# Kernel tuning notes

Measured on AMD Instinct MI355X. Metric: run time of the kernel, lower is better.

Reference implementation:

```python
import jax, jax.numpy as jnp
import numpy as np

# Hyperparameters (from __init__ defaults)
TIME_RES = 25
BASE_RES = 512
MAX_RES = 32768
N_LEVELS = 8
N_FEATS = 4
LOG2_HASHMAP = 13
HASHMAP_SIZE = 1 << LOG2_HASHMAP  # 8192
PRIME_Y = np.uint32(2654435761)   # instant-ngp 2D hash prime (dim0 prime is 1)

# Per-level grid scales (tcnn convention: scale = 2^(l*log2_pls)*base - 1)
_LOG2_PLS = np.log2(MAX_RES / BASE_RES) / (N_LEVELS - 1)
SCALES = jnp.asarray(np.exp2(np.arange(N_LEVELS) * _LOG2_PLS) * BASE_RES - 1.0,
                     dtype=jnp.float32)  # [L]


def _hash_encode(x, table_t):
    """Instant-NGP 2D multires hash encoding for one time slice.
    x: [N,2] in [0,1); table_t: [L, H, F]. Returns [N, L*F].
    All levels satisfy res^2 > HASHMAP_SIZE, so always the hash path."""
    N = x.shape[0]
    pos = x[:, None, :] * SCALES[None, :, None] + 0.5        # [N,L,2]
    pos_i = jnp.floor(pos)
    frac = pos - pos_i                                        # [N,L,2]
    pos_i = pos_i.astype(jnp.uint32)
    lvl = jnp.arange(N_LEVELS, dtype=jnp.int32)[None, :]      # [1,L]
    acc = jnp.zeros((N, N_LEVELS, N_FEATS), dtype=table_t.dtype)
    mask = jnp.uint32(HASHMAP_SIZE - 1)
    for dx in (0, 1):  # 4 bilinear corners (static unroll)
        for dy in (0, 1):
            ix = pos_i[..., 0] + jnp.uint32(dx)               # [N,L]
            iy = pos_i[..., 1] + jnp.uint32(dy)
            h = jnp.bitwise_xor(ix, iy * PRIME_Y) & mask      # [N,L] hash index
            w = (frac[..., 0] if dx else 1.0 - frac[..., 0]) * \
                (frac[..., 1] if dy else 1.0 - frac[..., 1])  # [N,L]
            f = table_t[lvl, h.astype(jnp.int32)]             # [N,L,F] gather
            acc = acc + w[..., None] * f
    return acc.reshape(N, N_LEVELS * N_FEATS)


def setup_inputs() -> dict:
    key = jax.random.key(0)
    k1, k2 = jax.random.split(key)
    N = 2_000_000
    x = jax.random.uniform(k1, (N, 2), dtype=jnp.float32)
    t = jnp.asarray(0.3, dtype=jnp.float32)  # scalar time in [0,1]
    # tcnn initializes hash tables uniform in [-1e-4, 1e-4]
    table = jax.random.uniform(k2, (TIME_RES, N_LEVELS, HASHMAP_SIZE, N_FEATS),
                               dtype=jnp.float32, minval=-1e-4, maxval=1e-4)
    return {"x": x, "t": t, "table": table}


def reference(x, t, table):
    idx = t * (TIME_RES - 1)
    i1 = jnp.floor(idx).astype(jnp.int32)
    i2 = jnp.ceil(idx).astype(jnp.int32)
    # blend weight; equals (i2-idx, idx-i1) when i1!=i2 and (1,0) when equal,
    # matching the torch branch semantics.
    w2 = idx - i1.astype(idx.dtype)
    w1 = 1.0 - w2
    tab1 = jax.lax.dynamic_index_in_dim(table, i1, axis=0, keepdims=False)
    tab2 = jax.lax.dynamic_index_in_dim(table, i2, axis=0, keepdims=False)
    f1 = _hash_encode(x, tab1)  # [N, 32]
    f2 = _hash_encode(x, tab2)
    return w1 * f1 + w2 * f2
```

## Files before the change

### kernel.cpp

```cpp
#include <hip/hip_runtime.h>
#include <hip/hip_fp16.h>
#include <math.h>

#define NLV 8
#define NF 4
#define HSZ 8192
#define TRES 25
#define PRIME 2654435761u

struct Scales { float s[NLV]; };

__global__ __launch_bounds__(256) void blend_kernel(
    const float* __restrict__ table, const float* __restrict__ tptr,
    __half2* __restrict__ bt)
{
    int i = blockIdx.x * 256 + threadIdx.x;
    float t = *tptr;
    float idx = t * (float)(TRES - 1);
    float fi1 = floorf(idx);
    float fi2 = ceilf(idx);
    float w2 = idx - fi1;
    float w1 = 1.0f - w2;
    size_t off1 = (size_t)(int)fi1 * (size_t)(NLV * HSZ * NF);
    size_t off2 = (size_t)(int)fi2 * (size_t)(NLV * HSZ * NF);
    float4 a = ((const float4*)(table + off1))[i];
    float4 b = ((const float4*)(table + off2))[i];
    float4 r;
    r.x = w1 * a.x + w2 * b.x;
    r.y = w1 * a.y + w2 * b.y;
    r.z = w1 * a.z + w2 * b.z;
    r.w = w1 * a.w + w2 * b.w;
    int l = i >> 13;
    int h = i & (HSZ - 1);
    bt[(size_t)l * 16384 + h]        = __floats2half2_rn(r.x, r.y);
    bt[(size_t)l * 16384 + 8192 + h] = __floats2half2_rn(r.z, r.w);
}

__global__ __launch_bounds__(1024) void encode_kernel(
    const float* __restrict__ x, const float4* __restrict__ bt,
    float* __restrict__ out, int npts, Scales sc)
{
    extern __shared__ __half2 smem[];
    int tid = threadIdx.x;
    int n0 = blockIdx.x * 1024 + tid;
    int n = n0 < npts ? n0 : npts - 1;
    float2 p = ((const float2*)x)[n];

    float4 acc[NLV];

    #pragma unroll
    for (int l = 0; l < NLV; ++l) {
        const float4* src = bt + (size_t)l * 4096;
        float4* dst = (float4*)smem;
        #pragma unroll
        for (int k = 0; k < 4; ++k) dst[tid + k * 1024] = src[tid + k * 1024];
        __syncthreads();

        float scale = sc.s[l];
        float px = __fadd_rn(__fmul_rn(p.x, scale), 0.5f);
        float py = __fadd_rn(__fmul_rn(p.y, scale), 0.5f);
        float fx0 = floorf(px), fy0 = floorf(py);
        float fx = px - fx0, fy = py - fy0;
        unsigned ix = (unsigned)(int)fx0;
        unsigned iy = (unsigned)(int)fy0;
        unsigned hy0 = iy * PRIME;
        unsigned hy1 = hy0 + PRIME;
        unsigned h00 = (ix         ^ hy0) & (HSZ - 1);
        unsigned h01 = (ix         ^ hy1) & (HSZ - 1);
        unsigned h10 = ((ix + 1u)  ^ hy0) & (HSZ - 1);
        unsigned h11 = ((ix + 1u)  ^ hy1) & (HSZ - 1);

        const __half2* t0 = smem;
        const __half2* t1 = smem + 8192;
        float2 a00 = __half22float2(t0[h00]), b00 = __half22float2(t1[h00]);
        float2 a01 = __half22float2(t0[h01]), b01 = __half22float2(t1[h01]);
        float2 a10 = __half22float2(t0[h10]), b10 = __half22float2(t1[h10]);
        float2 a11 = __half22float2(t0[h11]), b11 = __half22float2(t1[h11]);

        float gx = 1.0f - fx, gy = 1.0f - fy;
        float w00 = gx * gy, w01 = gx * fy, w10 = fx * gy, w11 = fx * fy;

        float4 r;
        r.x = w00 * a00.x + w01 * a01.x + w10 * a10.x + w11 * a11.x;
        r.y = w00 * a00.y + w01 * a01.y + w10 * a10.y + w11 * a11.y;
        r.z = w00 * b00.x + w01 * b01.x + w10 * b10.x + w11 * b11.x;
        r.w = w00 * b00.y + w01 * b01.y + w10 * b10.y + w11 * b11.y;
        acc[l] = r;
        __syncthreads();
    }

    if (n0 < npts) {
        float4* o = (float4*)(out + (size_t)n0 * 32);
        #pragma unroll
        for (int l = 0; l < NLV; ++l) o[l] = acc[l];
    }
}

extern "C" void kernel_launch(void* const* d_in, const int* in_sizes, int n_in,
                              void* d_out, int out_size, void* d_ws, size_t ws_size,
                              hipStream_t stream) {
    const float* x     = (const float*)d_in[0];
    const float* t     = (const float*)d_in[1];
    const float* table = (const float*)d_in[2];
    float* out = (float*)d_out;
    __half2* bt = (__half2*)d_ws;

    int npts = in_sizes[0] / 2;

    Scales sc;
    const double l2p = log2(32768.0 / 512.0) / 7.0;
    for (int l = 0; l < NLV; ++l)
        sc.s[l] = (float)(exp2((double)l * l2p) * 512.0 - 1.0);

    blend_kernel<<<(NLV * HSZ) / 256, 256, 0, stream>>>(table, t, bt);

    int nblocks = (npts + 1023) / 1024;
    encode_kernel<<<nblocks, 1024, 64 * 1024, stream>>>(
        x, (const float4*)bt, out, npts, sc);
}
```

Before: 397.3 us.

## Process four points per thread with double-buffered interleaved LDS table

Each block now handles 4096 points, with each thread computing four points. The per-level table staged in LDS is reused across four times more points, cutting global/L2 reloads of the table. The level tables are double-buffered so the next level's global loads overlap the current gathers, leaving one barrier per level. The blend output is interleaved so each corner fetch is a single 8-byte LDS read. The 128KB static shared footprint limits occupancy to one block per CU and raises register pressure.

```diff
diff --git a/kernel.cpp b/kernel.cpp
--- a/kernel.cpp
+++ b/kernel.cpp
@@ -30,69 +30,116 @@
     r.y = w1 * a.y + w2 * b.y;
     r.z = w1 * a.z + w2 * b.z;
     r.w = w1 * a.w + w2 * b.w;
-    int l = i >> 13;
-    int h = i & (HSZ - 1);
-    bt[(size_t)l * 16384 + h]        = __floats2half2_rn(r.x, r.y);
-    bt[(size_t)l * 16384 + 8192 + h] = __floats2half2_rn(r.z, r.w);
+    bt[2 * (size_t)i]     = __floats2half2_rn(r.x, r.y);
+    bt[2 * (size_t)i + 1] = __floats2half2_rn(r.z, r.w);
 }
 
-__global__ __launch_bounds__(1024) void encode_kernel(
+__device__ __forceinline__ float2 h2f(unsigned u) {
+    return __half22float2(__builtin_bit_cast(__half2, u));
+}
+
+__device__ __forceinline__ float4 gather_lvl(const uint2* tbl, float2 p, float scale)
+{
+    float px = __fadd_rn(__fmul_rn(p.x, scale), 0.5f);
+    float py = __fadd_rn(__fmul_rn(p.y, scale), 0.5f);
+    float fx0 = floorf(px), fy0 = floorf(py);
+    float fx = px - fx0, fy = py - fy0;
+    unsigned ix = (unsigned)(int)fx0;
+    unsigned iy = (unsigned)(int)fy0;
+    unsigned hy0 = iy * PRIME;
+    unsigned hy1 = hy0 + PRIME;
+    unsigned h00 = (ix         ^ hy0) & (HSZ - 1);
+    unsigned h01 = (ix         ^ hy1) & (HSZ - 1);
+    unsigned h10 = ((ix + 1u)  ^ hy0) & (HSZ - 1);
+    unsigned h11 = ((ix + 1u)  ^ hy1) & (HSZ - 1);
+    uint2 v00 = tbl[h00];
+    uint2 v01 = tbl[h01];
+    uint2 v10 = tbl[h10];
+    uint2 v11 = tbl[h11];
+    float gx = 1.0f - fx, gy = 1.0f - fy;
+    float w00 = gx * gy, w01 = gx * fy, w10 = fx * gy, w11 = fx * fy;
+    float2 a00 = h2f(v00.x), b00 = h2f(v00.y);
+    float2 a01 = h2f(v01.x), b01 = h2f(v01.y);
+    float2 a10 = h2f(v10.x), b10 = h2f(v10.y);
+    float2 a11 = h2f(v11.x), b11 = h2f(v11.y);
+    float4 r;
+    r.x = w00 * a00.x + w01 * a01.x + w10 * a10.x + w11 * a11.x;
+    r.y = w00 * a00.y + w01 * a01.y + w10 * a10.y + w11 * a11.y;
+    r.z = w00 * b00.x + w01 * b01.x + w10 * b10.x + w11 * b11.x;
+    r.w = w00 * b00.y + w01 * b01.y + w10 * b10.y + w11 * b11.y;
+    return r;
+}
+
+__global__ __launch_bounds__(1024, 4) void encode_kernel(
     const float* __restrict__ x, const float4* __restrict__ bt,
     float* __restrict__ out, int npts, Scales sc)
 {
-    extern __shared__ __half2 smem[];
+    __shared__ float4 smem[2][4096];
     int tid = threadIdx.x;
-    int n0 = blockIdx.x * 1024 + tid;
-    int n = n0 < npts ? n0 : npts - 1;
-    float2 p = ((const float2*)x)[n];
+    int base = blockIdx.x * 4096 + tid;
+    int n0 = base, n1 = base + 1024, n2 = base + 2048, n3 = base + 3072;
+    int c0 = n0 < npts ? n0 : npts - 1;
+    int c1 = n1 < npts ? n1 : npts - 1;
+    int c2 = n2 < npts ? n2 : npts - 1;
+    int c3 = n3 < npts ? n3 : npts - 1;
+    float2 p0 = ((const float2*)x)[c0];
+    float2 p1 = ((const float2*)x)[c1];
+    float2 p2 = ((const float2*)x)[c2];
+    float2 p3 = ((const float2*)x)[c3];
 
-    float4 acc[NLV];
+    float4 acc[4][4];
+
+    {
+        const float4* src = bt;
+        float4 s0 = src[tid], s1 = src[tid + 1024],
+               s2 = src[tid + 2048], s3 = src[tid + 3072];
+        smem[0][tid] = s0; smem[0][tid + 1024] = s1;
+        smem[0][tid + 2048] = s2; smem[0][tid + 3072] = s3;
+    }
+    __syncthreads();
 
     #pragma unroll
     for (int l = 0; l < NLV; ++l) {
-        const float4* src = bt + (size_t)l * 4096;
-        float4* dst = (float4*)smem;
-        #pragma unroll
-        for (int k = 0; k < 4; ++k) dst[tid + k * 1024] = src[tid + k * 1024];
+        float4 s0, s1, s2, s3;
+        if (l < NLV - 1) {
+            const float4* src = bt + (size_t)(l + 1) * 4096;
+            s0 = src[tid];        s1 = src[tid + 1024];
+            s2 = src[tid + 2048]; s3 = src[tid + 3072];
+        }
+
+        const uint2* tbl = (const uint2*)smem[l & 1];
+        float scale = sc.s[l];
+        acc[0][l & 3] = gather_lvl(tbl, p0, scale);
+        acc[1][l & 3] = gather_lvl(tbl, p1, scale);
+        acc[2][l & 3] = gather_lvl(tbl, p2, scale);
+        acc[3][l & 3] = gather_lvl(tbl, p3, scale);
+
+        if (l < NLV - 1) {
+            float4* dst = smem[(l & 1) ^ 1];
+            dst[tid] = s0; dst[tid + 1024] = s1;
+            dst[tid + 2048] = s2; dst[tid + 3072] = s3;
+        }
+
+        if ((l & 3) == 3) {
+            int g = l >> 2;
+            if (n0 < npts) {
+                float4* o = (float4*)(out + (size_t)n0 * 32) + g * 4;
+                o[0] = acc[0][0]; o[1] = acc[0][1]; o[2] = acc[0][2]; o[3] = acc[0][3];
+            }
+            if (n1 < npts) {
+                float4* o = (float4*)(out + (size_t)n1 * 32) + g * 4;
+                o[0] = acc[1][0]; o[1] = acc[1][1]; o[2] = acc[1][2]; o[3] = acc[1][3];
+            }
+            if (n2 < npts) {
+                float4* o = (float4*)(out + (size_t)n2 * 32) + g * 4;
+                o[0] = acc[2][0]; o[1] = acc[2][1]; o[2] = acc[2][2]; o[3] = acc[2][3];
+            }
+            if (n3 < npts) {
+                float4* o = (float4*)(out + (size_t)n3 * 32) + g * 4;
+                o[0] = acc[3][0]; o[1] = acc[3][1]; o[2] = acc[3][2]; o[3] = acc[3][3];
+            }
+        }
         __syncthreads();
-
-        float scale = sc.s[l];
-        float px = __fadd_rn(__fmul_rn(p.x, scale), 0.5f);
-        float py = __fadd_rn(__fmul_rn(p.y, scale), 0.5f);
-        float fx0 = floorf(px), fy0 = floorf(py);
-        float fx = px - fx0, fy = py - fy0;
-        unsigned ix = (unsigned)(int)fx0;
-        unsigned iy = (unsigned)(int)fy0;
-        unsigned hy0 = iy * PRIME;
-        unsigned hy1 = hy0 + PRIME;
-        unsigned h00 = (ix         ^ hy0) & (HSZ - 1);
-        unsigned h01 = (ix         ^ hy1) & (HSZ - 1);
-        unsigned h10 = ((ix + 1u)  ^ hy0) & (HSZ - 1);
-        unsigned h11 = ((ix + 1u)  ^ hy1) & (HSZ - 1);
-
-        const __half2* t0 = smem;
-        const __half2* t1 = smem + 8192;
-        float2 a00 = __half22float2(t0[h00]), b00 = __half22float2(t1[h00]);
-        float2 a01 = __half22float2(t0[h01]), b01 = __half22float2(t1[h01]);
-        float2 a10 = __half22float2(t0[h10]), b10 = __half22float2(t1[h10]);
-        float2 a11 = __half22float2(t0[h11]), b11 = __half22float2(t1[h11]);
-
-        float gx = 1.0f - fx, gy = 1.0f - fy;
-        float w00 = gx * gy, w01 = gx * fy, w10 = fx * gy, w11 = fx * fy;
-
-        float4 r;
-        r.x = w00 * a00.x + w01 * a01.x + w10 * a10.x + w11 * a11.x;
-        r.y = w00 * a00.y + w01 * a01.y + w10 * a10.y + w11 * a11.y;
-        r.z = w00 * b00.x + w01 * b01.x + w10 * b10.x + w11 * b11.x;
-        r.w = w00 * b00.y + w01 * b01.y + w10 * b10.y + w11 * b11.y;
-        acc[l] = r;
-        __syncthreads();
-    }
-
-    if (n0 < npts) {
-        float4* o = (float4*)(out + (size_t)n0 * 32);
-        #pragma unroll
-        for (int l = 0; l < NLV; ++l) o[l] = acc[l];
     }
 }
 
@@ -114,7 +161,7 @@
 
     blend_kernel<<<(NLV * HSZ) / 256, 256, 0, stream>>>(table, t, bt);
 
-    int nblocks = (npts + 1023) / 1024;
-    encode_kernel<<<nblocks, 1024, 64 * 1024, stream>>>(
+    int nblocks = (npts + 4095) / 4096;
+    encode_kernel<<<nblocks, 1024, 0, stream>>>(
         x, (const float4*)bt, out, npts, sc);
 }
```

Measured after the change: 460.7 us. 1.16x slower.
